# Kernel tuning notes

Hardware: AMD Instinct MI355X
Metric: run time of the kernel (lower is better)

Reference implementation:

```python
import jax, jax.numpy as jnp
import numpy as np


def setup_inputs() -> dict:
    key = jax.random.key(0)
    k1, k2 = jax.random.split(key)
    x = jax.random.normal(k1, (16, 256, 4096), dtype=jnp.float32)          # [B, D, T]
    codebooks = jax.random.normal(k2, (8, 1024, 256), dtype=jnp.float32)   # [n_q, bins, D]
    return {"x": x, "codebooks": codebooks}


def _quantize_one(residual, embed):
    """residual: [B, T, D]; embed: [bins, D] -> (quantize [B,T,D], idx [B,T])."""
    # negative squared euclidean distance (encodec euclidean codebook)
    x_sq = jnp.sum(residual * residual, axis=-1, keepdims=True)            # [B, T, 1]
    e_sq = jnp.sum(embed * embed, axis=-1)                                  # [bins]
    dots = jnp.einsum("btd,nd->btn", residual, embed)                       # [B, T, bins]
    dist = -(x_sq - 2.0 * dots + e_sq)                                      # [B, T, bins]
    idx = jnp.argmax(dist, axis=-1)                                         # [B, T] int
    quantize = embed[idx]                                                   # gather [B, T, D]
    return quantize, idx


def reference(x, codebooks):
    """Residual VQ forward (inference path, EMA updates omitted).
    x: [B, D, T]; codebooks: [n_q, bins, D].
    Returns (quantized [B, D, T], codes [n_q, B, T]).
    """
    n_q = codebooks.shape[0]
    residual = jnp.transpose(x, (0, 2, 1))                                  # [B, T, D]
    quantized_out = jnp.zeros_like(residual)
    codes = []
    for q in range(n_q):  # small fixed structural loop over quantizer stages
        quantize, idx = _quantize_one(residual, codebooks[q])
        # straight-through estimator as in encodec VectorQuantization
        quantize = residual + jax.lax.stop_gradient(quantize - residual)
        residual = residual - quantize
        quantized_out = quantized_out + quantize
        codes.append(idx)
    quantized = jnp.transpose(quantized_out, (0, 2, 1))                     # [B, D, T]
    codes = jnp.stack(codes, axis=0)                                        # [n_q, B, T]
    return quantized, codes
```

## Files before the change

### kernel.cpp

```cpp
#include <hip/hip_runtime.h>


#define BB   16
#define DD   256
#define TT   4096
#define NQ   8
#define BINS 1024
#define DELTA 4.0f
#define SOFF  8192.0f
#define OUTQ ((size_t)BB * DD * TT)

typedef _Float16 half8 __attribute__((ext_vector_type(8)));
typedef float    facc  __attribute__((ext_vector_type(4)));

#define MFMA16(A, B, C) __builtin_amdgcn_mfma_f32_16x16x32_f16((A), (B), (C), 0, 0, 0)

__global__ __launch_bounds__(256)
void rvq_pack_h16(const float* __restrict__ cb, _Float16* __restrict__ pks) {
    int gid = blockIdx.x * 256 + threadIdx.x;
    int s   = gid & 7;
    int bin = (gid >> 3) & 1023;
    int q   = gid >> 13;
    const float* src = cb + ((size_t)(q * BINS + bin)) * DD + s * 32;
    int cc    = q * 64 + (bin >> 4);
    int c     = bin & 15;
    size_t base = (size_t)cc * 4096 + (size_t)s * 512 + c * 8;
    #pragma unroll
    for (int g = 0; g < 4; ++g) {
        float4 v0 = *(const float4*)(src + g * 8);
        float4 v1 = *(const float4*)(src + g * 8 + 4);
        float vv[8] = { v0.x, v0.y, v0.z, v0.w, v1.x, v1.y, v1.z, v1.w };
        half8 h8;
        #pragma unroll
        for (int j = 0; j < 8; ++j) h8[j] = (_Float16)vv[j];
        *(half8*)&pks[base + g * 128] = h8;
    }
}

__global__ __launch_bounds__(256)
void rvq_esq_off(const float* __restrict__ cb, float* __restrict__ hoff) {
    int q = blockIdx.x;
    const float* e = cb + (size_t)q * BINS * DD;
    for (int bin = threadIdx.x; bin < BINS; bin += 256) {
        const float4* row = (const float4*)(e + (size_t)bin * DD);
        float s = 0.f;
        #pragma unroll 8
        for (int i = 0; i < DD / 4; ++i) {
            float4 v = row[i];
            s += v.x * v.x + v.y * v.y + v.z * v.z + v.w * v.w;
        }
        hoff[q * BINS + bin] = SOFF - 8.0f * s;
    }
}

__global__ __launch_bounds__(256, 2)
void rvq_mfma11_kernel(const float* __restrict__ x, const float* __restrict__ cb,
                       const _Float16* __restrict__ pks, const float* __restrict__ hoff,
                       float* __restrict__ out)
{
    __shared__ float esq_lds[BINS];
    __shared__ unsigned short best_lds[4][32];
    __shared__ unsigned short hist_lds[4][NQ][32];

    const int tid = threadIdx.x;
    const int w   = tid >> 6;
    const int l   = tid & 63;
    const int c   = l & 15;
    const int g   = l >> 4;

    const int blk = blockIdx.x;
    const int b   = blk >> 5;
    const int t0  = (blk & 31) * 128;
    const int tw  = t0 + w * 32;

    const char* pkbase = (const char*)pks + ((l >> 4) * 256 + (l & 15) * 16);

    half8 rh[2][8], rl[2][8];
    {
        const float* xb = x + (size_t)b * DD * TT;
        #pragma unroll
        for (int s = 0; s < 8; ++s) {
            #pragma unroll
            for (int j = 0; j < 8; ++j) {
                int d = s * 32 + g * 8 + j;
                #pragma unroll
                for (int m = 0; m < 2; ++m) {
                    int t = tw + m * 16 + c;
                    float v = 16.0f * xb[(size_t)d * TT + t];
                    _Float16 h = (_Float16)v;
                    rh[m][s][j] = h;
                    rl[m][s][j] = (_Float16)(v - (float)h);
                }
            }
        }
    }
    {
        float4 v = *(const float4*)(hoff + tid * 4);
        *(float4*)&esq_lds[tid * 4] = v;
    }
    __syncthreads();

    float p1[2][4], p2[2][4], p3[2][4];

    half8 Bx[8], By[8];

#define LOADB(BSET, K) do {                                                  \
    const char* _src = pkbase + (size_t)(K) * 8192;                          \
    _Pragma("unroll")                                                        \
    for (int _s = 0; _s < 8; ++_s)                                           \
        BSET[_s] = *(const half8*)(_src + _s * 1024);                        \
} while (0)

#define COMPUTE(BSET, CH) do {                                               \
    facc _a0 = {0.f,0.f,0.f,0.f}, _a1 = {0.f,0.f,0.f,0.f};                   \
    _Pragma("unroll")                                                        \
    for (int _s = 0; _s < 8; ++_s) {                                         \
        _a0 = MFMA16(rh[0][_s], BSET[_s], _a0);                              \
        _a1 = MFMA16(rh[1][_s], BSET[_s], _a1);                              \
    }                                                                        \
    const float _q0 = esq_lds[(CH) * 16 + c];                                \
    const unsigned _idx0 = 1023u - (unsigned)((CH) * 16 + c);                \
    _Pragma("unroll")                                                        \
    for (int _fm = 0; _fm < 2; ++_fm) {                                      \
        _Pragma("unroll")                                                    \
        for (int _fj = 0; _fj < 4; ++_fj) {                                  \
            float _sv = (_fm ? _a1[_fj] : _a0[_fj]) + _q0;                   \
            float _v = __builtin_bit_cast(float,                            \
                         (__builtin_bit_cast(unsigned, _sv) & ~1023u) | _idx0); \
            float _o1 = p1[_fm][_fj], _o2 = p2[_fm][_fj], _o3 = p3[_fm][_fj]; \
            p1[_fm][_fj] = fmaxf(_o1, _v);                                   \
            p2[_fm][_fj] = __builtin_amdgcn_fmed3f(_v, _o1, _o2);            \
            p3[_fm][_fj] = __builtin_amdgcn_fmed3f(_v, _o2, _o3);            \
        }                                                                    \
    }                                                                        \
} while (0)

    auto refine3 = [&](int tkl, int qq, int c1, int c2, int c3) -> int {
        int t = tw + tkl;
        double pa = 0.0, pb = 0.0, pc = 0.0;
        const float* e1p = cb + (size_t)(qq * BINS + c1) * DD;
        const float* e2p = cb + (size_t)(qq * BINS + c2) * DD;
        const float* e3p = cb + (size_t)(qq * BINS + c3) * DD;
        #pragma unroll
        for (int dd = 0; dd < 4; ++dd) {
            int d = l * 4 + dd;
            float rv = x[((size_t)b * DD + d) * TT + t];
            for (int k = 0; k < qq; ++k) {
                int hb = hist_lds[w][k][tkl];
                rv -= cb[(size_t)(k * BINS + hb) * DD + d];
            }
            float e1v = e1p[d], e2v = e2p[d], e3v = e3p[d];
            pa += (double)e1v * (2.0 * (double)rv - (double)e1v);
            pb += (double)e2v * (2.0 * (double)rv - (double)e2v);
            pc += (double)e3v * (2.0 * (double)rv - (double)e3v);
        }
        #pragma unroll
        for (int mk = 1; mk < 64; mk <<= 1) {
            pa += __shfl_xor(pa, mk);
            pb += __shfl_xor(pb, mk);
            pc += __shfl_xor(pc, mk);
        }
        int wbin = c1; double pw = pa;
        if (pb > pw || (pb == pw && c2 < wbin)) { pw = pb; wbin = c2; }
        if (pc > pw || (pc == pw && c3 < wbin)) { pw = pc; wbin = c3; }
        return wbin;
    };

    auto stage_end = [&](int qq) {
        int  bch[2][4], cn2[2][4], cn3[2][4];
        bool gate[2][4];
        #pragma unroll
        for (int fm = 0; fm < 2; ++fm) {
            #pragma unroll
            for (int fj = 0; fj < 4; ++fj) {
                float a1 = p1[fm][fj], a2 = p2[fm][fj], a3 = p3[fm][fj];
                #pragma unroll
                for (int mk = 1; mk < 16; mk <<= 1) {
                    float b1 = __shfl_xor(a1, mk);
                    float b2 = __shfl_xor(a2, mk);
                    float b3 = __shfl_xor(a3, mk);
                    float lo1 = fminf(a1, b1);
                    float m22 = fmaxf(a2, b2);
                    float r1  = fmaxf(a1, b1);
                    float r2  = fmaxf(lo1, m22);
                    float r3  = fmaxf(fminf(lo1, m22), fmaxf(fminf(a2, b2), fmaxf(a3, b3)));
                    a1 = r1; a2 = r2; a3 = r3;
                }
                bch[fm][fj] = 1023 - (int)(__builtin_bit_cast(unsigned, a1) & 1023u);
                cn2[fm][fj] = 1023 - (int)(__builtin_bit_cast(unsigned, a2) & 1023u);
                cn3[fm][fj] = 1023 - (int)(__builtin_bit_cast(unsigned, a3) & 1023u);
                gate[fm][fj] = (a1 - a2 <= DELTA);
            }
        }
        bool anyg = gate[0][0] | gate[0][1] | gate[0][2] | gate[0][3]
                  | gate[1][0] | gate[1][1] | gate[1][2] | gate[1][3];
        if (__any(anyg)) {
            #pragma unroll
            for (int fm = 0; fm < 2; ++fm) {
                #pragma unroll
                for (int fj = 0; fj < 4; ++fj) {
                    unsigned long long nm = __ballot(gate[fm][fj]);
                    if (nm) {
                        for (int g2 = 0; g2 < 4; ++g2) {
                            if ((nm >> (g2 * 16)) & 1ull) {
                                int c1 = __shfl(bch[fm][fj], g2 * 16);
                                int c2 = __shfl(cn2[fm][fj], g2 * 16);
                                int c3 = __shfl(cn3[fm][fj], g2 * 16);
                                int tkl = fm * 16 + g2 * 4 + fj;
                                int wb = refine3(tkl, qq, c1, c2, c3);
                                if (g == g2) bch[fm][fj] = wb;
                            }
                        }
                    }
                }
            }
        }

        if (c == 0) {
            #pragma unroll
            for (int fm = 0; fm < 2; ++fm)
                #pragma unroll
                for (int fj = 0; fj < 4; ++fj) {
                    int tkl = fm * 16 + g * 4 + fj;
                    best_lds[w][tkl] = (unsigned short)bch[fm][fj];
                    hist_lds[w][qq][tkl] = (unsigned short)bch[fm][fj];
                    out[OUTQ + ((size_t)qq * BB + b) * TT + tw + tkl] = (float)bch[fm][fj];
                }
        }

        #pragma unroll
        for (int m = 0; m < 2; ++m) {
            int bin = best_lds[w][m * 16 + c];
            const float* ep = cb + (size_t)(qq * BINS + bin) * DD + g * 8;
            #pragma unroll
            for (int s = 0; s < 8; ++s) {
                float4 e0 = *(const float4*)(ep + s * 32);
                float4 e1 = *(const float4*)(ep + s * 32 + 4);
                float ev[8] = { e0.x, e0.y, e0.z, e0.w, e1.x, e1.y, e1.z, e1.w };
                #pragma unroll
                for (int j = 0; j < 8; ++j) {
                    float rv = (float)rh[m][s][j] + (float)rl[m][s][j];
                    float nr = rv - 16.0f * ev[j];
                    _Float16 nh = (_Float16)nr;
                    rh[m][s][j] = nh;
                    rl[m][s][j] = (_Float16)(nr - (float)nh);
                }
            }
        }
    };

    #pragma unroll 1
    for (int q = 0; q < NQ; ++q) {
        #pragma unroll
        for (int fm = 0; fm < 2; ++fm)
            #pragma unroll
            for (int fj = 0; fj < 4; ++fj) {
                p1[fm][fj] = 0.f; p2[fm][fj] = 0.f; p3[fm][fj] = 0.f;
            }
        const int base = q * 64;
        LOADB(Bx, base + 0);
        #pragma unroll 1
        for (int p = 0; p < 32; ++p) {
            const int ch = 2 * p;
            LOADB(By, base + ch + 1);
            COMPUTE(Bx, ch);
            if (p < 31) LOADB(Bx, base + ch + 2);
            COMPUTE(By, ch + 1);
        }
        stage_end(q);
        __syncthreads();
        if (q + 1 < NQ) {
            float4 v = *(const float4*)(hoff + (q + 1) * BINS + tid * 4);
            *(float4*)&esq_lds[tid * 4] = v;
        }
        __syncthreads();
    }

    {
        const float* xb = x + (size_t)b * DD * TT;
        float* ob = out + (size_t)b * DD * TT;
        #pragma unroll
        for (int s = 0; s < 8; ++s)
            #pragma unroll
            for (int j = 0; j < 8; ++j) {
                int d = s * 32 + g * 8 + j;
                #pragma unroll
                for (int m = 0; m < 2; ++m) {
                    int t = tw + m * 16 + c;
                    float rv = ((float)rh[m][s][j] + (float)rl[m][s][j]) * 0.0625f;
                    ob[(size_t)d * TT + t] = xb[(size_t)d * TT + t] - rv;
                }
            }
    }
}

#define TOK_PER_BLK 32
#define BIN_CHUNK   128
#define KC          32
#define EPAD        36
#define RPAD        260
#define FDELTA      0.0078125f

#define FUPD2(S, BIN, B1, I1, B2, I2)                                        \
    if ((S) > (B2) || ((S) == (B2) && (BIN) < (I2))) {                      \
        if ((S) > (B1) || ((S) == (B1) && (BIN) < (I1))) {                  \
            B2 = B1; I2 = I1; B1 = (S); I1 = (BIN);                         \
        } else { B2 = (S); I2 = (BIN); }                                    \
    }

__global__ __launch_bounds__(256, 2)
void rvq_esq_kernel(const float* __restrict__ cb, float* __restrict__ esq) {
    int q = blockIdx.x;
    const float* e = cb + (size_t)q * BINS * DD;
    for (int bin = threadIdx.x; bin < BINS; bin += 256) {
        const float4* row = (const float4*)(e + (size_t)bin * DD);
        float s = 0.f;
        #pragma unroll 8
        for (int i = 0; i < DD / 4; ++i) {
            float4 v = row[i];
            s += v.x * v.x + v.y * v.y + v.z * v.z + v.w * v.w;
        }
        esq[q * BINS + bin] = s;
    }
}

__global__ __launch_bounds__(256, 2)
void rvq_main_kernel(const float* __restrict__ x, const float* __restrict__ cb,
                     const float* __restrict__ esq, float* __restrict__ out) {
    __shared__ float r_lds[TOK_PER_BLK][RPAD];
    __shared__ float e_lds[BIN_CHUNK][EPAD];
    __shared__ float red_s[16][2][TOK_PER_BLK];
    __shared__ int   red_i[16][2][TOK_PER_BLK];
    __shared__ int   best_lds2[TOK_PER_BLK];

    const int tid = threadIdx.x;
    const int blk = blockIdx.x;
    const int b   = blk >> 7;
    const int t0  = (blk & 127) * TOK_PER_BLK;

    {
        const int tl = tid & 31;
        const int d0 = (tid >> 5) * 32;
        const float* xp = x + (size_t)b * DD * TT + t0 + tl;
        for (int dd = 0; dd < 32; ++dd) {
            int d = d0 + dd;
            r_lds[tl][d] = xp[(size_t)d * TT];
        }
    }
    __syncthreads();

    const int ty = tid >> 4;
    const int tx = tid & 15;

    for (int q = 0; q < NQ; ++q) {
        const float* eb = cb + (size_t)q * BINS * DD;
        const float* es = esq + q * BINS;
        float b1[2] = {-1e30f, -1e30f}, b2[2] = {-1e30f, -1e30f};
        int   i1[2] = {0x7fffffff, 0x7fffffff}, i2[2] = {0x7fffffff, 0x7fffffff};

        for (int cch = 0; cch < BINS / BIN_CHUNK; ++cch) {
            float acc[2][8];
            #pragma unroll
            for (int i = 0; i < 2; ++i)
                #pragma unroll
                for (int j = 0; j < 8; ++j) acc[i][j] = 0.f;

            for (int kc = 0; kc < DD / KC; ++kc) {
                __syncthreads();
                {
                    const int col  = tid & 7;
                    const int row0 = tid >> 3;
                    const float* src = eb + (size_t)(cch * BIN_CHUNK) * DD + kc * KC;
                    #pragma unroll
                    for (int rr = 0; rr < 4; ++rr) {
                        int row = row0 + rr * 32;
                        float4 v = *(const float4*)(src + (size_t)row * DD + col * 4);
                        *(float4*)&e_lds[row][col * 4] = v;
                    }
                }
                __syncthreads();
                #pragma unroll
                for (int k4 = 0; k4 < KC / 4; ++k4) {
                    float4 r0 = *(const float4*)&r_lds[tx][kc * KC + k4 * 4];
                    float4 r1 = *(const float4*)&r_lds[tx + 16][kc * KC + k4 * 4];
                    #pragma unroll
                    for (int bi = 0; bi < 8; ++bi) {
                        float4 e4 = *(const float4*)&e_lds[ty + 16 * bi][k4 * 4];
                        acc[0][bi] += r0.x * e4.x + r0.y * e4.y + r0.z * e4.z + r0.w * e4.w;
                        acc[1][bi] += r1.x * e4.x + r1.y * e4.y + r1.z * e4.z + r1.w * e4.w;
                    }
                }
            }
            #pragma unroll
            for (int bi = 0; bi < 8; ++bi) {
                int bin = cch * BIN_CHUNK + ty + 16 * bi;
                float half_esq = 0.5f * es[bin];
                float s0 = acc[0][bi] - half_esq;
                float s1v = acc[1][bi] - half_esq;
                FUPD2(s0, bin, b1[0], i1[0], b2[0], i2[0]);
                FUPD2(s1v, bin, b1[1], i1[1], b2[1], i2[1]);
            }
        }

        #pragma unroll
        for (int k = 0; k < 2; ++k) {
            red_s[ty][k][tx]      = k ? b2[0] : b1[0];
            red_i[ty][k][tx]      = k ? i2[0] : i1[0];
            red_s[ty][k][tx + 16] = k ? b2[1] : b1[1];
            red_i[ty][k][tx + 16] = k ? i2[1] : i1[1];
        }
        __syncthreads();

        if (tid < TOK_PER_BLK) {
            float g1 = -1e30f, g2 = -1e30f; int gi1 = 0x7fffffff, gi2 = 0x7fffffff;
            #pragma unroll
            for (int j = 0; j < 16; ++j) {
                #pragma unroll
                for (int k = 0; k < 2; ++k) {
                    float s = red_s[j][k][tid]; int ii = red_i[j][k][tid];
                    FUPD2(s, ii, g1, gi1, g2, gi2);
                }
            }
            int bif;
            if (g1 - g2 <= FDELTA) {
                const float* rrow = r_lds[tid];
                double sc[2]; int id2[2] = { gi1, gi2 };
                for (int cc2 = 0; cc2 < 2; ++cc2) {
                    const float* ep = eb + (size_t)id2[cc2] * DD;
                    double acc2 = 0.0;
                    #pragma unroll 4
                    for (int d = 0; d < DD; ++d) {
                        double ev = (double)ep[d];
                        acc2 += ev * (2.0 * (double)rrow[d] - ev);
                    }
                    sc[cc2] = acc2;
                }
                bif = (sc[0] > sc[1] || (sc[0] == sc[1] && id2[0] < id2[1])) ? id2[0] : id2[1];
            } else {
                bif = gi1;
            }
            best_lds2[tid] = bif;
            out[OUTQ + (size_t)q * (BB * TT) + (size_t)b * TT + t0 + tid] = (float)bif;
        }
        __syncthreads();

        {
            const int tok  = tid >> 3;
            const int part = tid & 7;
            const int bin  = best_lds2[tok];
            const float* ep = eb + (size_t)bin * DD + part * 32;
            float* rp = &r_lds[tok][part * 32];
            #pragma unroll
            for (int dd = 0; dd < 32; ++dd) rp[dd] -= ep[dd];
        }
        __syncthreads();
    }

    {
        const int tl = tid & 31;
        const int d0 = (tid >> 5) * 32;
        const float* xp = x + (size_t)b * DD * TT + t0 + tl;
        float*       op = out + (size_t)b * DD * TT + t0 + tl;
        for (int dd = 0; dd < 32; ++dd) {
            int d = d0 + dd;
            op[(size_t)d * TT] = xp[(size_t)d * TT] - r_lds[tl][d];
        }
    }
}

extern "C" void kernel_launch(void* const* d_in, const int* in_sizes, int n_in,
                              void* d_out, int out_size, void* d_ws, size_t ws_size,
                              hipStream_t stream) {
    const float* x  = (const float*)d_in[0];
    const float* cb = (const float*)d_in[1];
    float* out = (float*)d_out;

    const size_t PKS_BYTES = (size_t)NQ * BINS * DD * 2;
    const size_t NEED = PKS_BYTES + (size_t)NQ * BINS * 4;

    if (ws_size >= NEED) {
        _Float16* pks = (_Float16*)d_ws;
        float* hoff = (float*)((char*)d_ws + PKS_BYTES);
        rvq_pack_h16<<<(NQ * BINS * 8) / 256, 256, 0, stream>>>(cb, pks);
        rvq_esq_off<<<NQ, 256, 0, stream>>>(cb, hoff);
        rvq_mfma11_kernel<<<512, 256, 0, stream>>>(x, cb, pks, hoff, out);
    } else {
        float* esq = (float*)d_ws;
        rvq_esq_kernel<<<NQ, 256, 0, stream>>>(cb, esq);
        rvq_main_kernel<<<(BB * TT) / TOK_PER_BLK, 256, 0, stream>>>(x, cb, esq, out);
    }
}
```

Before: 622.9 us.

## Move residual low-half fp16 registers to LDS and triple-buffer codebook loads

The low-order fp16 half of the split residual, previously held in 64 registers per thread, now lives in shared memory and is read and written only during the per-stage residual update and the final output. The freed registers fund a third B-fragment buffer, so the inner distance loop runs with a deeper prefetch of three codebook chunks in flight. The aim is to hide global load latency in the MFMA loop without raising register pressure, at the cost of 64 KB of extra LDS per block, which may limit how many blocks fit per CU.

```diff
diff --git a/kernel.cpp b/kernel.cpp
--- a/kernel.cpp
+++ b/kernel.cpp
@@ -54,11 +54,12 @@
 }
 
 __global__ __launch_bounds__(256, 2)
-void rvq_mfma11_kernel(const float* __restrict__ x, const float* __restrict__ cb,
+void rvq_mfma12_kernel(const float* __restrict__ x, const float* __restrict__ cb,
                        const _Float16* __restrict__ pks, const float* __restrict__ hoff,
                        float* __restrict__ out)
 {
     __shared__ float esq_lds[BINS];
+    __shared__ half8 rl_lds[2][8][4][64];
     __shared__ unsigned short best_lds[4][32];
     __shared__ unsigned short hist_lds[4][NQ][32];
 
@@ -75,7 +76,7 @@
 
     const char* pkbase = (const char*)pks + ((l >> 4) * 256 + (l & 15) * 16);
 
-    half8 rh[2][8], rl[2][8];
+    half8 rh[2][8];
     {
         const float* xb = x + (size_t)b * DD * TT;
         #pragma unroll
@@ -89,8 +90,22 @@
                     float v = 16.0f * xb[(size_t)d * TT + t];
                     _Float16 h = (_Float16)v;
                     rh[m][s][j] = h;
-                    rl[m][s][j] = (_Float16)(v - (float)h);
-                }
+                }
+            }
+        }
+        #pragma unroll
+        for (int s = 0; s < 8; ++s) {
+            #pragma unroll
+            for (int m = 0; m < 2; ++m) {
+                int t = tw + m * 16 + c;
+                half8 rlv;
+                #pragma unroll
+                for (int j = 0; j < 8; ++j) {
+                    int d = s * 32 + g * 8 + j;
+                    float v = 16.0f * xb[(size_t)d * TT + t];
+                    rlv[j] = (_Float16)(v - (float)rh[m][s][j]);
+                }
+                rl_lds[m][s][w][l] = rlv;
             }
         }
     }
@@ -102,7 +117,7 @@
 
     float p1[2][4], p2[2][4], p3[2][4];
 
-    half8 Bx[8], By[8];
+    half8 Bx[8], By[8], Bz[8];
 
 #define LOADB(BSET, K) do {                                                  \
     const char* _src = pkbase + (size_t)(K) * 8192;                          \
@@ -237,14 +252,17 @@
                 float4 e0 = *(const float4*)(ep + s * 32);
                 float4 e1 = *(const float4*)(ep + s * 32 + 4);
                 float ev[8] = { e0.x, e0.y, e0.z, e0.w, e1.x, e1.y, e1.z, e1.w };
+                half8 rlv = rl_lds[m][s][w][l];
+                half8 nrl;
                 #pragma unroll
                 for (int j = 0; j < 8; ++j) {
-                    float rv = (float)rh[m][s][j] + (float)rl[m][s][j];
+                    float rv = (float)rh[m][s][j] + (float)rlv[j];
                     float nr = rv - 16.0f * ev[j];
                     _Float16 nh = (_Float16)nr;
                     rh[m][s][j] = nh;
-                    rl[m][s][j] = (_Float16)(nr - (float)nh);
-                }
+                    nrl[j] = (_Float16)(nr - (float)nh);
+                }
+                rl_lds[m][s][w][l] = nrl;
             }
         }
     };
@@ -259,14 +277,19 @@
             }
         const int base = q * 64;
         LOADB(Bx, base + 0);
+        LOADB(By, base + 1);
+        LOADB(Bz, base + 2);
         #pragma unroll 1
-        for (int p = 0; p < 32; ++p) {
-            const int ch = 2 * p;
-            LOADB(By, base + ch + 1);
+        for (int pp = 0; pp < 21; ++pp) {
+            const int ch = 3 * pp;
             COMPUTE(Bx, ch);
-            if (p < 31) LOADB(Bx, base + ch + 2);
+            LOADB(Bx, base + ch + 3);
             COMPUTE(By, ch + 1);
-        }
+            if (ch + 4 < 64) LOADB(By, base + ch + 4);
+            COMPUTE(Bz, ch + 2);
+            if (ch + 5 < 64) LOADB(Bz, base + ch + 5);
+        }
+        COMPUTE(Bx, 63);
         stage_end(q);
         __syncthreads();
         if (q + 1 < NQ) {
@@ -280,17 +303,21 @@
         const float* xb = x + (size_t)b * DD * TT;
         float* ob = out + (size_t)b * DD * TT;
         #pragma unroll
-        for (int s = 0; s < 8; ++s)
+        for (int s = 0; s < 8; ++s) {
+            half8 rl0 = rl_lds[0][s][w][l];
+            half8 rl1 = rl_lds[1][s][w][l];
             #pragma unroll
             for (int j = 0; j < 8; ++j) {
                 int d = s * 32 + g * 8 + j;
                 #pragma unroll
                 for (int m = 0; m < 2; ++m) {
                     int t = tw + m * 16 + c;
-                    float rv = ((float)rh[m][s][j] + (float)rl[m][s][j]) * 0.0625f;
+                    float rlv = (float)(m ? rl1[j] : rl0[j]);
+                    float rv = ((float)rh[m][s][j] + rlv) * 0.0625f;
                     ob[(size_t)d * TT + t] = xb[(size_t)d * TT + t] - rv;
                 }
             }
+        }
     }
 }
 
@@ -483,7 +510,7 @@
         float* hoff = (float*)((char*)d_ws + PKS_BYTES);
         rvq_pack_h16<<<(NQ * BINS * 8) / 256, 256, 0, stream>>>(cb, pks);
         rvq_esq_off<<<NQ, 256, 0, stream>>>(cb, hoff);
-        rvq_mfma11_kernel<<<512, 256, 0, stream>>>(x, cb, pks, hoff, out);
+        rvq_mfma12_kernel<<<512, 256, 0, stream>>>(x, cb, pks, hoff, out);
     } else {
         float* esq = (float*)d_ws;
         rvq_esq_kernel<<<NQ, 256, 0, stream>>>(cb, esq);
```

After: 585.4 us. -6.0%, faster.
